# Kernel optimization log

Hardware: AMD Instinct MI355X
Metric: run time of the kernel (lower is better)

The kernel has to match this reference:

```python
import jax, jax.numpy as jnp
import numpy as np

NUM_HEADS = 16
THETA = 10000.0
B, S, D = 2, 2048, 1024
D_K = D // NUM_HEADS


def setup_inputs() -> dict:
    key = jax.random.key(0)
    ks = jax.random.split(key, 5)
    s = 0.02
    return {
        "x": jax.random.normal(ks[0], (B, S, D), dtype=jnp.float32),
        "W_q": jax.random.normal(ks[1], (D, D), dtype=jnp.float32) * s,
        "W_k": jax.random.normal(ks[2], (D, D), dtype=jnp.float32) * s,
        "W_v": jax.random.normal(ks[3], (D, D), dtype=jnp.float32) * s,
        "W_o": jax.random.normal(ks[4], (D, D), dtype=jnp.float32) * s,
        "token_positions": jnp.arange(S, dtype=jnp.int32),
    }


def _rope(x, token_positions):
    # x: [..., seq, d_k]; equivalent to the block-diagonal 2x2 rotation matmul
    d2 = x.shape[-1] // 2
    inv_freq = THETA ** (-(2.0 * jnp.arange(d2, dtype=x.dtype)) / x.shape[-1])  # [d2]
    ang = token_positions.astype(x.dtype)[:, None] * inv_freq[None, :]  # [seq, d2]
    cos, sin = jnp.cos(ang), jnp.sin(ang)
    xp = x.reshape(x.shape[:-1] + (d2, 2))
    xe, xo = xp[..., 0], xp[..., 1]
    oe = cos * xe - sin * xo
    oo = sin * xe + cos * xo
    return jnp.stack([oe, oo], axis=-1).reshape(x.shape)


def reference(x, W_q, W_k, W_v, W_o, token_positions):
    seq = x.shape[-2]
    # QKV projections (weights stored as [out, in])
    Q = jnp.einsum('bsd,ed->bse', x, W_q)
    K = jnp.einsum('bsd,ed->bse', x, W_k)
    V = jnp.einsum('bsd,ed->bse', x, W_v)
    def split_heads(t):
        return t.reshape(t.shape[:-1] + (NUM_HEADS, D_K)).swapaxes(-3, -2)  # [b,h,s,dk]
    Q, K, V = split_heads(Q), split_heads(K), split_heads(V)
    Q = _rope(Q, token_positions)
    K = _rope(K, token_positions)
    scale = 1.0 / np.sqrt(D_K)
    scores = jnp.einsum('bhqd,bhkd->bhqk', Q, K) * scale
    causal = jnp.tril(jnp.ones((seq, seq), dtype=bool))
    scores = jnp.where(causal, scores, -jnp.inf)
    probs = jax.nn.softmax(scores, axis=-1)
    out = jnp.einsum('bhqk,bhkd->bhqd', probs, V)
    out = out.swapaxes(-3, -2).reshape(x.shape[:-1] + (D,))
    return jnp.einsum('bse,de->bsd', out, W_o)
```

## Files before the change

kernel.cpp:

```cpp
#include <hip/hip_runtime.h>
#include <hip/hip_bf16.h>
#include <math.h>

#define H_    16
#define DK_   64
#define Dm    1024
#define Bb    2
#define Ss    2048
#define Mrows 4096
#define QSCALE 0.1803368801f

typedef short s16x8 __attribute__((ext_vector_type(8)));
typedef float f32x4 __attribute__((ext_vector_type(4)));
typedef unsigned short u16;
typedef unsigned int u32;

__device__ __forceinline__ u16 f2b(float f) {
  __hip_bfloat16 h = __float2bfloat16(f);
  return *reinterpret_cast<u16*>(&h);
}
__device__ __forceinline__ float b2f(u16 u) {
  __hip_bfloat16 h;
  *reinterpret_cast<u16*>(&h) = u;
  return __bfloat162float(h);
}
__device__ __forceinline__ u32 pkbf(float hi, float lo) {
  return __builtin_amdgcn_perm(__float_as_uint(hi), __float_as_uint(lo), 0x07060302u);
}

#define GLDS(g, l)                                                             \
  __builtin_amdgcn_global_load_lds(                                            \
      (const __attribute__((address_space(1))) unsigned int*)(g),              \
      (__attribute__((address_space(3))) unsigned int*)(l), 16, 0, 0)

__device__ __forceinline__ int SW64(int row, int col) {
  return row * 64 + ((((col >> 3) ^ (row & 7) ^ (row >> 3)) & 7) << 3) + (col & 7);
}

__global__ __launch_bounds__(256) void k_castall(
    const float* __restrict__ x,  const float* __restrict__ Wq,
    const float* __restrict__ Wk, const float* __restrict__ Wv,
    const float* __restrict__ Wo,
    u16* __restrict__ xb,  u16* __restrict__ wqb, u16* __restrict__ wkb,
    u16* __restrict__ wvb, u16* __restrict__ wob,
    const int* __restrict__ pos, float2* __restrict__ tab) {
  if (blockIdx.x >= 8192) {
    int t = (blockIdx.x - 8192) * 256 + threadIdx.x;
    int s = t >> 5, i = t & 31;
    float p = (float)pos[s];
    float ang = p * powf(10000.0f, -(float)i / 32.0f);
    tab[t] = make_float2(cosf(ang), sinf(ang));
    return;
  }
  int i = blockIdx.x * 256 + threadIdx.x;
  const float* s;
  u16* d;
  int off;
  if (i < 1048576) { s = x; d = xb; off = i; }
  else {
    int j = i - 1048576;
    int w = j >> 18;
    off = j & 262143;
    s = (w == 0) ? Wq : (w == 1) ? Wk : (w == 2) ? Wv : Wo;
    d = (w == 0) ? wqb : (w == 1) ? wkb : (w == 2) ? wvb : wob;
  }
  float4 v = reinterpret_cast<const float4*>(s)[off];
  ushort4 o;
  o.x = f2b(v.x); o.y = f2b(v.y); o.z = f2b(v.z); o.w = f2b(v.w);
  reinterpret_cast<ushort4*>(d)[off] = o;
}

__global__ __launch_bounds__(256) void k_ropeK(u16* __restrict__ K,
                                               const float2* __restrict__ tab) {
  int t = blockIdx.x * 256 + threadIdx.x;
  int row = t >> 7;
  int c0 = (t & 127) << 3;
  int i0 = (c0 & 63) >> 1;
  const float2* tb = &tab[(row & (Ss - 1)) * 32 + i0];
  float2 cs[4];
#pragma unroll
  for (int j = 0; j < 4; ++j) cs[j] = tb[j];
  size_t off = (size_t)row * Dm + c0;
  s16x8 k = *reinterpret_cast<const s16x8*>(&K[off]);
  s16x8 ko;
#pragma unroll
  for (int j = 0; j < 4; ++j) {
    float ke = b2f((u16)k[2 * j]), kd = b2f((u16)k[2 * j + 1]);
    ko[2 * j]     = (short)f2b(cs[j].x * ke - cs[j].y * kd);
    ko[2 * j + 1] = (short)f2b(cs[j].y * ke + cs[j].x * kd);
  }
  *reinterpret_cast<s16x8*>(&K[off]) = ko;
}

template <int BN, bool QKV>
__global__ __launch_bounds__(256) void k_gemm(
    const u16* __restrict__ A, const u16* __restrict__ B,
    u16* __restrict__ OQ, u16* __restrict__ OK2, u16* __restrict__ OVT,
    float* __restrict__ OF, int K) {
  constexpr int NFR = BN / 32;
  __shared__ __align__(16) u16 lsA[3][128 * 32];
  __shared__ __align__(16) u16 lsB[3][BN * 32];
  const int tid = threadIdx.x, lane = tid & 63, wave = tid >> 6;
  const int quad = lane >> 4, l16 = lane & 15;
  const int wrow = wave >> 1, wcol = wave & 1;
  const int n0 = blockIdx.x * BN, m0 = blockIdx.y * 128;
  f32x4 acc[4][NFR] = {};

  auto stage = [&](int k0, int bi) {
#pragma unroll
    for (int c = 0; c < 2; ++c) {
      int f = (wave * 2 + c) * 64 + lane;
      int row = f >> 2;
      int gs = (f & 3) ^ ((row >> 1) & 3);
      GLDS(A + (size_t)(m0 + row) * K + k0 + gs * 8, &lsA[bi][(wave * 2 + c) * 512]);
    }
#pragma unroll
    for (int c = 0; c < NFR / 2; ++c) {
      int f = (wave * (NFR / 2) + c) * 64 + lane;
      int row = f >> 2;
      int gs = (f & 3) ^ ((row >> 1) & 3);
      GLDS(B + (size_t)(n0 + row) * K + k0 + gs * 8, &lsB[bi][(wave * (NFR / 2) + c) * 512]);
    }
  };

  stage(0, 0);
  stage(32, 1);
  int bi = 0, stg = 2;
  for (int k0 = 0; k0 < K; k0 += 32) {
    if (k0 + 32 < K) {
      if constexpr (NFR == 4) asm volatile("s_waitcnt vmcnt(4)" ::: "memory");
      else                    asm volatile("s_waitcnt vmcnt(3)" ::: "memory");
    } else {
      asm volatile("s_waitcnt vmcnt(0)" ::: "memory");
    }
    __builtin_amdgcn_sched_barrier(0);
    __builtin_amdgcn_s_barrier();
    if (k0 + 64 < K) stage(k0 + 64, stg);
    s16x8 af[4], bfr[NFR];
#pragma unroll
    for (int i = 0; i < 4; ++i) {
      int row = wrow * 64 + i * 16 + l16;
      af[i] = *reinterpret_cast<const s16x8*>(
          &lsA[bi][row * 32 + ((quad ^ ((row >> 1) & 3)) << 3)]);
    }
#pragma unroll
    for (int i = 0; i < NFR; ++i) {
      int row = wcol * (BN / 2) + i * 16 + l16;
      bfr[i] = *reinterpret_cast<const s16x8*>(
          &lsB[bi][row * 32 + ((quad ^ ((row >> 1) & 3)) << 3)]);
    }
#pragma unroll
    for (int mi = 0; mi < 4; ++mi)
#pragma unroll
      for (int ni = 0; ni < NFR; ++ni)
        acc[mi][ni] = __builtin_amdgcn_mfma_f32_16x16x32_bf16(af[mi], bfr[ni], acc[mi][ni], 0, 0, 0);
    stg = bi;
    bi = (bi == 2) ? 0 : bi + 1;
  }

  if (QKV) {
    const int which = n0 >> 10;
    const int nbase = (n0 & 1023) + wcol * (BN / 2);
    if (which == 2) {
#pragma unroll
      for (int mi = 0; mi < 4; ++mi)
#pragma unroll
        for (int ni = 0; ni < NFR; ++ni) {
          int row0 = m0 + wrow * 64 + mi * 16 + quad * 4;
          int col  = nbase + ni * 16 + l16;
          int bb = row0 >> 11, s0 = row0 & (Ss - 1);
          ushort4 pk;
          pk.x = f2b(acc[mi][ni][0]); pk.y = f2b(acc[mi][ni][1]);
          pk.z = f2b(acc[mi][ni][2]); pk.w = f2b(acc[mi][ni][3]);
          *reinterpret_cast<ushort4*>(&OVT[((size_t)bb * Dm + col) * Ss + s0]) = pk;
        }
    } else {
      u16* Op = which ? OK2 : OQ;
#pragma unroll
      for (int mi = 0; mi < 4; ++mi)
#pragma unroll
        for (int ni = 0; ni < NFR; ++ni)
#pragma unroll
          for (int r = 0; r < 4; ++r) {
            int row = m0 + wrow * 64 + mi * 16 + quad * 4 + r;
            int col = nbase + ni * 16 + l16;
            Op[(size_t)row * Dm + col] = f2b(acc[mi][ni][r]);
          }
    }
  } else {
#pragma unroll
    for (int mi = 0; mi < 4; ++mi)
#pragma unroll
      for (int ni = 0; ni < NFR; ++ni)
#pragma unroll
        for (int r = 0; r < 4; ++r) {
          int row = m0 + wrow * 64 + mi * 16 + quad * 4 + r;
          int col = n0 + wcol * (BN / 2) + ni * 16 + l16;
          OF[(size_t)row * Dm + col] = acc[mi][ni][r];
        }
  }
}

__global__ __launch_bounds__(256) void k_flash(const u16* __restrict__ Q,
                                               const u16* __restrict__ K,
                                               const u16* __restrict__ VT,
                                               u16* __restrict__ O,
                                               const float2* __restrict__ tab) {
  __shared__ __align__(16) u16 lsK[4][64 * 64];
  __shared__ __align__(16) u16 lsVT[4][64 * 64];
  __shared__ __align__(16) u16 lsP[4][32 * 64];
  const int tid = threadIdx.x, lane = tid & 63, wave = tid >> 6;
  const int quad = lane >> 4, l16 = lane & 15;
  const int bid = blockIdx.x;
  const int bh = bid & 31;
  const int h = bh & (H_ - 1), b = bh >> 4;
  const int g = bid >> 5, a = g & 7, bsel = g >> 3;
  const int qt = bsel ? (15 - a) : a;
  const int q0 = qt * 128;
  const int qbase = q0 + wave * 32;
  const int ktmax_w = (qbase + 31) >> 6;
  const int xorv = (l16 * 2) & 0xE;

  s16x8 qf[2][2];
#pragma unroll
  for (int s = 0; s < 2; ++s) {
    const int qpos = qbase + s * 16 + l16;
    const size_t qoff = (size_t)(b * Ss + qpos) * Dm + h * 64;
    s16x8 r0 = *reinterpret_cast<const s16x8*>(&Q[qoff + quad * 8]);
    s16x8 r1 = *reinterpret_cast<const s16x8*>(&Q[qoff + 32 + quad * 8]);
    const float2* tb = &tab[(qpos & (Ss - 1)) * 32];
#pragma unroll
    for (int kc = 0; kc < 2; ++kc) {
      s16x8 raw = kc ? r1 : r0;
#pragma unroll
      for (int p = 0; p < 4; ++p) {
        float2 cs = tb[kc * 16 + quad * 4 + p];
        float e = b2f((u16)raw[2 * p]), o = b2f((u16)raw[2 * p + 1]);
        qf[s][kc][2 * p]     = (short)f2b((cs.x * e - cs.y * o) * QSCALE);
        qf[s][kc][2 * p + 1] = (short)f2b((cs.y * e + cs.x * o) * QSCALE);
      }
    }
  }
  s16x8 ones;
#pragma unroll
  for (int j = 0; j < 8; ++j) ones[j] = (short)0x3F80;

  f32x4 ot[2][4] = {};
  f32x4 lAcc[2] = {};

  auto stagepair = [&](int pp) {
#pragma unroll
    for (int half = 0; half < 2; ++half) {
      const int kt = pp * 2 + half;
      const int slot = kt & 3;
      const size_t kbase  = (size_t)(b * Ss + kt * 64) * Dm + h * 64;
      const size_t vtbase = ((size_t)b * Dm + h * 64) * Ss + kt * 64;
#pragma unroll
      for (int c = 0; c < 2; ++c) {
        int sl = (wave * 2 + c) * 64 + lane;
        int row = sl >> 3;
        int gg = ((sl & 7) ^ (row & 7) ^ (row >> 3)) & 7;
        GLDS(K  + kbase  + (size_t)row * Dm + gg * 8, &lsK[slot][(wave * 2 + c) * 512]);
        GLDS(VT + vtbase + (size_t)row * Ss + gg * 8, &lsVT[slot][(wave * 2 + c) * 512]);
      }
    }
  };

  stagepair(0);
  for (int pp = 0; pp <= qt; ++pp) {
    __syncthreads();
    if (pp < qt) stagepair(pp + 1);
    const int kt0 = 2 * pp;

    f32x4 st[2][2][4] = {};
#pragma unroll
    for (int half = 0; half < 2; ++half) {
      const int kt = kt0 + half;
      if (kt > ktmax_w) break;
      const int slot = kt & 3;
#pragma unroll
      for (int kc = 0; kc < 2; ++kc)
#pragma unroll
        for (int ni = 0; ni < 4; ++ni) {
          s16x8 kf = *reinterpret_cast<const s16x8*>(
              &lsK[slot][SW64(ni * 16 + l16, kc * 32 + quad * 8)]);
          st[half][0][ni] = __builtin_amdgcn_mfma_f32_16x16x32_bf16(kf, qf[0][kc], st[half][0][ni], 0, 0, 0);
          st[half][1][ni] = __builtin_amdgcn_mfma_f32_16x16x32_bf16(kf, qf[1][kc], st[half][1][ni], 0, 0, 0);
        }
    }
#pragma unroll
    for (int half = 0; half < 2; ++half) {
      const int kt = kt0 + half;
      if (kt > ktmax_w) break;
      const int slot = kt & 3;
      if (kt == ktmax_w) {
#pragma unroll
        for (int s = 0; s < 2; ++s) {
          int gq = qbase + s * 16 + l16;
#pragma unroll
          for (int ni = 0; ni < 4; ++ni)
#pragma unroll
            for (int r = 0; r < 4; ++r)
              if (kt * 64 + ni * 16 + quad * 4 + r > gq) st[half][s][ni][r] = -INFINITY;
        }
      }
#pragma unroll
      for (int s = 0; s < 2; ++s)
#pragma unroll
        for (int ni = 0; ni < 4; ++ni) {
          float e0 = __builtin_amdgcn_exp2f(st[half][s][ni][0]);
          float e1 = __builtin_amdgcn_exp2f(st[half][s][ni][1]);
          float e2 = __builtin_amdgcn_exp2f(st[half][s][ni][2]);
          float e3 = __builtin_amdgcn_exp2f(st[half][s][ni][3]);
          uint2 pk;
          pk.x = pkbf(e1, e0);
          pk.y = pkbf(e3, e2);
          *reinterpret_cast<uint2*>(
              &lsP[wave][(s * 16 + l16) * 64 + (((ni * 4 + quad) ^ xorv) << 2)]) = pk;
        }
#pragma unroll
      for (int kc = 0; kc < 2; ++kc) {
        s16x8 pf0 = *reinterpret_cast<const s16x8*>(
            &lsP[wave][l16 * 64 + (((kc * 8 + quad * 2) ^ xorv) << 2)]);
        s16x8 pf1 = *reinterpret_cast<const s16x8*>(
            &lsP[wave][(16 + l16) * 64 + (((kc * 8 + quad * 2) ^ xorv) << 2)]);
        lAcc[0] = __builtin_amdgcn_mfma_f32_16x16x32_bf16(ones, pf0, lAcc[0], 0, 0, 0);
        lAcc[1] = __builtin_amdgcn_mfma_f32_16x16x32_bf16(ones, pf1, lAcc[1], 0, 0, 0);
#pragma unroll
        for (int ni = 0; ni < 4; ++ni) {
          s16x8 vf = *reinterpret_cast<const s16x8*>(
              &lsVT[slot][SW64(ni * 16 + l16, kc * 32 + quad * 8)]);
          ot[0][ni] = __builtin_amdgcn_mfma_f32_16x16x32_bf16(vf, pf0, ot[0][ni], 0, 0, 0);
          ot[1][ni] = __builtin_amdgcn_mfma_f32_16x16x32_bf16(vf, pf1, ot[1][ni], 0, 0, 0);
        }
      }
    }
  }

#pragma unroll
  for (int s = 0; s < 2; ++s) {
    float inv = 1.0f / lAcc[s][0];
    const size_t obase = (size_t)(b * Ss + qbase + s * 16 + l16) * Dm + h * 64;
#pragma unroll
    for (int ni = 0; ni < 4; ++ni) {
      ushort4 pk;
      pk.x = f2b(ot[s][ni][0] * inv); pk.y = f2b(ot[s][ni][1] * inv);
      pk.z = f2b(ot[s][ni][2] * inv); pk.w = f2b(ot[s][ni][3] * inv);
      *reinterpret_cast<ushort4*>(&O[obase + ni * 16 + quad * 4]) = pk;
    }
  }
}

extern "C" void kernel_launch(void* const* d_in, const int* in_sizes, int n_in,
                              void* d_out, int out_size, void* d_ws, size_t ws_size,
                              hipStream_t stream) {
  const float* x  = (const float*)d_in[0];
  const float* Wq = (const float*)d_in[1];
  const float* Wk = (const float*)d_in[2];
  const float* Wv = (const float*)d_in[3];
  const float* Wo = (const float*)d_in[4];
  const int* pos  = (const int*)d_in[5];
  float* out = (float*)d_out;

  char* w = (char*)d_ws;
  u16* xb  = (u16*)w; w += (size_t)Mrows * Dm * 2;
  u16* wqb = (u16*)w; w += (size_t)Dm * Dm * 2;
  u16* wkb = (u16*)w; w += (size_t)Dm * Dm * 2;
  u16* wvb = (u16*)w; w += (size_t)Dm * Dm * 2;
  u16* wob = (u16*)w; w += (size_t)Dm * Dm * 2;
  u16* Qb  = (u16*)w; w += (size_t)Mrows * Dm * 2;
  u16* Kb  = (u16*)w; w += (size_t)Mrows * Dm * 2;
  u16* VTb = (u16*)w; w += (size_t)Mrows * Dm * 2;
  u16* Ab  = (u16*)w; w += (size_t)Mrows * Dm * 2;
  float2* tabf = (float2*)w; w += (size_t)Ss * 32 * sizeof(float2);

  k_castall<<<8448, 256, 0, stream>>>(x, Wq, Wk, Wv, Wo, xb, wqb, wkb, wvb, wob,
                                      pos, tabf);
  k_gemm<128, true><<<dim3(24, 32), 256, 0, stream>>>(xb, wqb, Qb, Kb, VTb, nullptr, Dm);
  k_ropeK<<<Mrows * Dm / 8 / 256, 256, 0, stream>>>(Kb, tabf);
  k_flash<<<dim3(512), 256, 0, stream>>>(Qb, Kb, VTb, Ab, tabf);
  k_gemm<64, false><<<dim3(16, 32), 256, 0, stream>>>(Ab, wob, nullptr, nullptr, nullptr, out, Dm);
}
```

Before: 186.2 us.

## Pipeline attention KV loads per tile with vmcnt waits and MFMA priority

```diff
diff --git a/kernel.cpp b/kernel.cpp
--- a/kernel.cpp
+++ b/kernel.cpp
@@ -48,7 +48,7 @@
     int t = (blockIdx.x - 8192) * 256 + threadIdx.x;
     int s = t >> 5, i = t & 31;
     float p = (float)pos[s];
-    float ang = p * powf(10000.0f, -(float)i / 32.0f);
+    float ang = p * __builtin_amdgcn_exp2f(-(float)i * 0.4152448120604907f);
     tab[t] = make_float2(cosf(ang), sinf(ang));
     return;
   }
@@ -248,92 +248,88 @@
   f32x4 ot[2][4] = {};
   f32x4 lAcc[2] = {};
 
-  auto stagepair = [&](int pp) {
-#pragma unroll
-    for (int half = 0; half < 2; ++half) {
-      const int kt = pp * 2 + half;
-      const int slot = kt & 3;
-      const size_t kbase  = (size_t)(b * Ss + kt * 64) * Dm + h * 64;
-      const size_t vtbase = ((size_t)b * Dm + h * 64) * Ss + kt * 64;
-#pragma unroll
-      for (int c = 0; c < 2; ++c) {
-        int sl = (wave * 2 + c) * 64 + lane;
-        int row = sl >> 3;
-        int gg = ((sl & 7) ^ (row & 7) ^ (row >> 3)) & 7;
-        GLDS(K  + kbase  + (size_t)row * Dm + gg * 8, &lsK[slot][(wave * 2 + c) * 512]);
-        GLDS(VT + vtbase + (size_t)row * Ss + gg * 8, &lsVT[slot][(wave * 2 + c) * 512]);
-      }
+  auto stage1 = [&](int kt) {
+    const int slot = kt & 3;
+    const size_t kbase  = (size_t)(b * Ss + kt * 64) * Dm + h * 64;
+    const size_t vtbase = ((size_t)b * Dm + h * 64) * Ss + kt * 64;
+#pragma unroll
+    for (int c = 0; c < 2; ++c) {
+      int sl = (wave * 2 + c) * 64 + lane;
+      int row = sl >> 3;
+      int gg = ((sl & 7) ^ (row & 7) ^ (row >> 3)) & 7;
+      GLDS(K  + kbase  + (size_t)row * Dm + gg * 8, &lsK[slot][(wave * 2 + c) * 512]);
+      GLDS(VT + vtbase + (size_t)row * Ss + gg * 8, &lsVT[slot][(wave * 2 + c) * 512]);
     }
   };
 
-  stagepair(0);
-  for (int pp = 0; pp <= qt; ++pp) {
-    __syncthreads();
-    if (pp < qt) stagepair(pp + 1);
-    const int kt0 = 2 * pp;
-
-    f32x4 st[2][2][4] = {};
-#pragma unroll
-    for (int half = 0; half < 2; ++half) {
-      const int kt = kt0 + half;
-      if (kt > ktmax_w) break;
-      const int slot = kt & 3;
-#pragma unroll
-      for (int kc = 0; kc < 2; ++kc)
-#pragma unroll
-        for (int ni = 0; ni < 4; ++ni) {
-          s16x8 kf = *reinterpret_cast<const s16x8*>(
-              &lsK[slot][SW64(ni * 16 + l16, kc * 32 + quad * 8)]);
-          st[half][0][ni] = __builtin_amdgcn_mfma_f32_16x16x32_bf16(kf, qf[0][kc], st[half][0][ni], 0, 0, 0);
-          st[half][1][ni] = __builtin_amdgcn_mfma_f32_16x16x32_bf16(kf, qf[1][kc], st[half][1][ni], 0, 0, 0);
-        }
-    }
-#pragma unroll
-    for (int half = 0; half < 2; ++half) {
-      const int kt = kt0 + half;
-      if (kt > ktmax_w) break;
-      const int slot = kt & 3;
-      if (kt == ktmax_w) {
-#pragma unroll
-        for (int s = 0; s < 2; ++s) {
-          int gq = qbase + s * 16 + l16;
-#pragma unroll
-          for (int ni = 0; ni < 4; ++ni)
-#pragma unroll
-            for (int r = 0; r < 4; ++r)
-              if (kt * 64 + ni * 16 + quad * 4 + r > gq) st[half][s][ni][r] = -INFINITY;
-        }
-      }
-#pragma unroll
-      for (int s = 0; s < 2; ++s)
-#pragma unroll
-        for (int ni = 0; ni < 4; ++ni) {
-          float e0 = __builtin_amdgcn_exp2f(st[half][s][ni][0]);
-          float e1 = __builtin_amdgcn_exp2f(st[half][s][ni][1]);
-          float e2 = __builtin_amdgcn_exp2f(st[half][s][ni][2]);
-          float e3 = __builtin_amdgcn_exp2f(st[half][s][ni][3]);
-          uint2 pk;
-          pk.x = pkbf(e1, e0);
-          pk.y = pkbf(e3, e2);
-          *reinterpret_cast<uint2*>(
-              &lsP[wave][(s * 16 + l16) * 64 + (((ni * 4 + quad) ^ xorv) << 2)]) = pk;
-        }
-#pragma unroll
-      for (int kc = 0; kc < 2; ++kc) {
-        s16x8 pf0 = *reinterpret_cast<const s16x8*>(
-            &lsP[wave][l16 * 64 + (((kc * 8 + quad * 2) ^ xorv) << 2)]);
-        s16x8 pf1 = *reinterpret_cast<const s16x8*>(
-            &lsP[wave][(16 + l16) * 64 + (((kc * 8 + quad * 2) ^ xorv) << 2)]);
-        lAcc[0] = __builtin_amdgcn_mfma_f32_16x16x32_bf16(ones, pf0, lAcc[0], 0, 0, 0);
-        lAcc[1] = __builtin_amdgcn_mfma_f32_16x16x32_bf16(ones, pf1, lAcc[1], 0, 0, 0);
-#pragma unroll
-        for (int ni = 0; ni < 4; ++ni) {
-          s16x8 vf = *reinterpret_cast<const s16x8*>(
-              &lsVT[slot][SW64(ni * 16 + l16, kc * 32 + quad * 8)]);
-          ot[0][ni] = __builtin_amdgcn_mfma_f32_16x16x32_bf16(vf, pf0, ot[0][ni], 0, 0, 0);
-          ot[1][ni] = __builtin_amdgcn_mfma_f32_16x16x32_bf16(vf, pf1, ot[1][ni], 0, 0, 0);
-        }
-      }
+  const int ktend = 2 * qt + 2;
+  stage1(0);
+  stage1(1);
+  for (int kt = 0; kt < ktend; ++kt) {
+    if (kt + 1 < ktend) asm volatile("s_waitcnt vmcnt(4)" ::: "memory");
+    else                asm volatile("s_waitcnt vmcnt(0)" ::: "memory");
+    __builtin_amdgcn_sched_barrier(0);
+    __builtin_amdgcn_s_barrier();
+    __builtin_amdgcn_sched_barrier(0);
+    if (kt + 2 < ktend) stage1(kt + 2);
+    if (kt > ktmax_w) continue;
+    const int slot = kt & 3;
+
+    f32x4 st[2][4] = {};
+    __builtin_amdgcn_s_setprio(1);
+#pragma unroll
+    for (int kc = 0; kc < 2; ++kc)
+#pragma unroll
+      for (int ni = 0; ni < 4; ++ni) {
+        s16x8 kf = *reinterpret_cast<const s16x8*>(
+            &lsK[slot][SW64(ni * 16 + l16, kc * 32 + quad * 8)]);
+        st[0][ni] = __builtin_amdgcn_mfma_f32_16x16x32_bf16(kf, qf[0][kc], st[0][ni], 0, 0, 0);
+        st[1][ni] = __builtin_amdgcn_mfma_f32_16x16x32_bf16(kf, qf[1][kc], st[1][ni], 0, 0, 0);
+      }
+    __builtin_amdgcn_s_setprio(0);
+
+    if (kt == ktmax_w) {
+#pragma unroll
+      for (int s = 0; s < 2; ++s) {
+        int gq = qbase + s * 16 + l16;
+#pragma unroll
+        for (int ni = 0; ni < 4; ++ni)
+#pragma unroll
+          for (int r = 0; r < 4; ++r)
+            if (kt * 64 + ni * 16 + quad * 4 + r > gq) st[s][ni][r] = -INFINITY;
+      }
+    }
+#pragma unroll
+    for (int s = 0; s < 2; ++s)
+#pragma unroll
+      for (int ni = 0; ni < 4; ++ni) {
+        float e0 = __builtin_amdgcn_exp2f(st[s][ni][0]);
+        float e1 = __builtin_amdgcn_exp2f(st[s][ni][1]);
+        float e2 = __builtin_amdgcn_exp2f(st[s][ni][2]);
+        float e3 = __builtin_amdgcn_exp2f(st[s][ni][3]);
+        uint2 pk;
+        pk.x = pkbf(e1, e0);
+        pk.y = pkbf(e3, e2);
+        *reinterpret_cast<uint2*>(
+            &lsP[wave][(s * 16 + l16) * 64 + (((ni * 4 + quad) ^ xorv) << 2)]) = pk;
+      }
+#pragma unroll
+    for (int kc = 0; kc < 2; ++kc) {
+      s16x8 pf0 = *reinterpret_cast<const s16x8*>(
+          &lsP[wave][l16 * 64 + (((kc * 8 + quad * 2) ^ xorv) << 2)]);
+      s16x8 pf1 = *reinterpret_cast<const s16x8*>(
+          &lsP[wave][(16 + l16) * 64 + (((kc * 8 + quad * 2) ^ xorv) << 2)]);
+      __builtin_amdgcn_s_setprio(1);
+      lAcc[0] = __builtin_amdgcn_mfma_f32_16x16x32_bf16(ones, pf0, lAcc[0], 0, 0, 0);
+      lAcc[1] = __builtin_amdgcn_mfma_f32_16x16x32_bf16(ones, pf1, lAcc[1], 0, 0, 0);
+#pragma unroll
+      for (int ni = 0; ni < 4; ++ni) {
+        s16x8 vf = *reinterpret_cast<const s16x8*>(
+            &lsVT[slot][SW64(ni * 16 + l16, kc * 32 + quad * 8)]);
+        ot[0][ni] = __builtin_amdgcn_mfma_f32_16x16x32_bf16(vf, pf0, ot[0][ni], 0, 0, 0);
+        ot[1][ni] = __builtin_amdgcn_mfma_f32_16x16x32_bf16(vf, pf1, ot[1][ni], 0, 0, 0);
+      }
+      __builtin_amdgcn_s_setprio(0);
     }
   }
 
```

Measured after the change: 190.7 us. +2.4%, slower.
